# Optimization experiments

Measured on AMD Instinct MI355X. Metric: run time of the kernel, lower is better.

The kernel has to match this reference:

```python
import jax, jax.numpy as jnp
import numpy as np

PALACE_N = 64   # base palace mask size
PALACE_BLOCK = 8  # 8 palaces of 8 positions each


def _palace_base():
    # base 64x64 mask: 1.0 within a palace (8x8 diagonal blocks), 0.5 across palaces
    pid = jnp.arange(PALACE_N) // PALACE_BLOCK
    intra = pid[:, None] == pid[None, :]
    return jnp.where(intra, 1.0, 0.5).astype(jnp.float32)


def _get_mask(T, inter_palace_weight):
    # tile base mask by index modulo 64 (matches mask[i % 64, j % 64])
    base = _palace_base()
    ii = jnp.arange(T) % PALACE_N
    base_T = base[ii[:, None], ii[None, :]]            # [T, T]
    intra = (base_T == 1.0).astype(jnp.float32)
    inter = (base_T < 1.0).astype(jnp.float32)
    return intra + jax.nn.sigmoid(inter_palace_weight) * inter


def setup_inputs() -> dict:
    key = jax.random.key(0)
    ks = jax.random.split(key, 5)
    B, T, D = 4, 2048, 1024
    x = jax.random.normal(ks[0], (B, T, D), dtype=jnp.float32)
    s = 1.0 / np.sqrt(D)
    Wq = jax.random.normal(ks[1], (D, D), dtype=jnp.float32) * s
    Wk = jax.random.normal(ks[2], (D, D), dtype=jnp.float32) * s
    Wv = jax.random.normal(ks[3], (D, D), dtype=jnp.float32) * s
    inter_palace_weight = jnp.float32(0.1)
    return {"x": x, "Wq": Wq, "Wk": Wk, "Wv": Wv,
            "inter_palace_weight": inter_palace_weight}


def reference(x, Wq, Wk, Wv, inter_palace_weight):
    B, T, D = x.shape
    H = 16
    hd = D // H
    scale = hd ** -0.5
    pmask = _get_mask(T, inter_palace_weight)          # [T, T]
    # torch Linear: x @ W.T
    q = (x @ Wq.T).reshape(B, T, H, hd)
    k = (x @ Wk.T).reshape(B, T, H, hd)
    v = (x @ Wv.T).reshape(B, T, H, hd)
    attn = jnp.einsum('bqhd,bkhd->bhqk', q, k) * scale
    attn = attn * pmask[None, None, :, :]
    attn = jax.nn.softmax(attn, axis=-1)
    attn = jnp.nan_to_num(attn, nan=0.0)
    out = jnp.einsum('bhqk,bkhd->bqhd', attn, v)
    return out.reshape(B, T, D)
```

## Files before the change

### kernel.cpp

```cpp
#include <hip/hip_runtime.h>

typedef unsigned short u16;
typedef unsigned int u32;
typedef short bf16x8 __attribute__((ext_vector_type(8)));
typedef float f32x4 __attribute__((ext_vector_type(4)));
typedef u32 u32x4 __attribute__((ext_vector_type(4)));

#define AS_GLOBAL __attribute__((address_space(1)))
#define AS_LDS __attribute__((address_space(3)))

__device__ __forceinline__ void async16(const void* g, void* l) {
  __builtin_amdgcn_global_load_lds((const AS_GLOBAL u32*)g, (AS_LDS u32*)l, 16, 0, 0);
}

__device__ __forceinline__ u16 f2bf(float f) {
  u32 u = __builtin_bit_cast(u32, f);
  u += 0x7FFFu + ((u >> 16) & 1u);
  return (u16)(u >> 16);
}

__device__ __forceinline__ u32 pk2bf(float lo, float hi) {
  return __builtin_amdgcn_perm(__builtin_bit_cast(u32, hi),
                               __builtin_bit_cast(u32, lo), 0x07060302u);
}

__device__ __forceinline__ float fexp2(float x) {
#if __has_builtin(__builtin_amdgcn_exp2f)
  return __builtin_amdgcn_exp2f(x);
#else
  return exp2f(x);
#endif
}

__global__ __launch_bounds__(256) void cvt_all(const float* __restrict__ x,
                                               const float* __restrict__ wq,
                                               const float* __restrict__ wk,
                                               const float* __restrict__ wv,
                                               u16* __restrict__ xb,
                                               u16* __restrict__ wb) {
  const int blk = blockIdx.x;
  const float* src;
  u16* dst;
  int i;
  if (blk < 8192) {
    src = x; dst = xb; i = blk * 256 + threadIdx.x;
  } else if (blk < 9216) {
    src = wq; dst = wb; i = (blk - 8192) * 256 + threadIdx.x;
  } else if (blk < 10240) {
    src = wk; dst = wb + 1048576; i = (blk - 9216) * 256 + threadIdx.x;
  } else {
    src = wv; dst = wb + 2097152; i = (blk - 10240) * 256 + threadIdx.x;
  }
  float4 f = reinterpret_cast<const float4*>(src)[i];
  ushort4 o;
  o.x = f2bf(f.x); o.y = f2bf(f.y); o.z = f2bf(f.z); o.w = f2bf(f.w);
  reinterpret_cast<ushort4*>(dst)[i] = o;
}

__global__ __launch_bounds__(256, 2) void qkv_gemm(const u16* __restrict__ X,
                                                   const u16* __restrict__ W,
                                                   u16* __restrict__ O) {
  const int z = blockIdx.z;
  const u16* Wz = W + (size_t)z * (1024 * 1024);
  u16* Oz = O + (size_t)z * (8192 * 1024);

  __shared__ __align__(16) u16 SMEM[4][8192];

  const int t = threadIdx.x;
  const int lane = t & 63, w = t >> 6, quad = lane >> 4, lq = lane & 15;
  const int wm = (w >> 1) * 64, wn = (w & 1) * 64;
  const int sw = lq & 7;
  const size_t m0 = (size_t)blockIdx.x * 128;
  const int n0 = blockIdx.y * 128;

  int off[4];
#pragma unroll
  for (int j = 0; j < 4; ++j) {
    const int s = j * 256 + t, row = s >> 3, c = (s & 7) ^ (row & 7);
    off[j] = row * 1024 + c * 8;
  }
  const u16* gA = X + m0 * 1024;
  const u16* gB = Wz + (size_t)n0 * 1024;

  f32x4 acc[4][4];
#pragma unroll
  for (int i = 0; i < 4; ++i)
#pragma unroll
    for (int j = 0; j < 4; ++j) acc[i][j] = f32x4{0.f, 0.f, 0.f, 0.f};

  auto stage = [&](int kt, int nb) {
    const u16* ga = gA + kt * 64;
    const u16* gb = gB + kt * 64;
#pragma unroll
    for (int j = 0; j < 4; ++j)
      async16(ga + off[j], &SMEM[nb][(j * 256 + t) * 8]);
#pragma unroll
    for (int j = 0; j < 4; ++j)
      async16(gb + off[j], &SMEM[2 + nb][(j * 256 + t) * 8]);
  };

  stage(0, 0);

  for (int kt = 0; kt < 16; ++kt) {
    const int cur = kt & 1;
    __syncthreads();
    if (kt < 15) stage(kt + 1, cur ^ 1);

    bf16x8 Af[4][2], Bf[4][2];
#pragma unroll
    for (int i = 0; i < 4; ++i)
#pragma unroll
      for (int ks = 0; ks < 2; ++ks) {
        Af[i][ks] = *reinterpret_cast<const bf16x8*>(
            &SMEM[cur][(wm + i * 16 + lq) * 64 + ((ks * 4 + quad) ^ sw) * 8]);
        Bf[i][ks] = *reinterpret_cast<const bf16x8*>(
            &SMEM[2 + cur][(wn + i * 16 + lq) * 64 + ((ks * 4 + quad) ^ sw) * 8]);
      }
#pragma unroll
    for (int i = 0; i < 4; ++i)
#pragma unroll
      for (int j = 0; j < 4; ++j) {
        acc[i][j] = __builtin_amdgcn_mfma_f32_16x16x32_bf16(Af[i][0], Bf[j][0], acc[i][j], 0, 0, 0);
        acc[i][j] = __builtin_amdgcn_mfma_f32_16x16x32_bf16(Af[i][1], Bf[j][1], acc[i][j], 0, 0, 0);
      }
  }

  __syncthreads();
  u16* ep = &SMEM[w][0];
  if (z != 2) {
#pragma unroll
    for (int i = 0; i < 4; ++i)
#pragma unroll
      for (int j = 0; j < 4; ++j)
#pragma unroll
        for (int r = 0; r < 4; ++r)
          ep[(i * 16 + quad * 4 + r) * 80 + j * 16 + lq] = f2bf(acc[i][j][r]);
  } else {
#pragma unroll
    for (int i = 0; i < 4; ++i)
#pragma unroll
      for (int j = 0; j < 4; ++j)
#pragma unroll
        for (int r = 0; r < 4; ++r)
          ep[(j * 16 + lq) * 80 + i * 16 + quad * 4 + r] = f2bf(acc[i][j][r]);
  }
  asm volatile("s_waitcnt lgkmcnt(0)" ::: "memory");

  const int r8 = lane >> 3, c8 = lane & 7;
  const size_t ms = m0 + wm;
  const size_t bb = ms >> 11, tt0 = ms & 2047;
  const int hh = (n0 + wn) >> 6;
  if (z != 2) {
    u16* gbase = Oz + ((bb * 16 + hh) * 2048 + tt0) * 64;
#pragma unroll
    for (int kq = 0; kq < 8; ++kq) {
      const int row = kq * 8 + r8;
      bf16x8 v = *reinterpret_cast<const bf16x8*>(&ep[row * 80 + c8 * 8]);
      *reinterpret_cast<bf16x8*>(&gbase[(size_t)row * 64 + c8 * 8]) = v;
    }
  } else {
    u16* gbase = Oz + ((size_t)(bb * 16 + hh) * 64) * 2048 + tt0;
#pragma unroll
    for (int kq = 0; kq < 8; ++kq) {
      const int row = kq * 8 + r8;
      bf16x8 v = *reinterpret_cast<const bf16x8*>(&ep[row * 80 + c8 * 8]);
      *reinterpret_cast<bf16x8*>(&gbase[(size_t)row * 2048 + c8 * 8]) = v;
    }
  }
}

__global__ __launch_bounds__(256, 2) void palace_attn(const u16* __restrict__ Q,
                                                      const u16* __restrict__ K,
                                                      const u16* __restrict__ Vt,
                                                      float* __restrict__ out,
                                                      const float* __restrict__ wptr) {
  const int bh = blockIdx.x, qt = blockIdx.y;
  const int h = bh & 15, b = bh >> 4;
  const size_t base = (size_t)bh * (2048 * 64);

  __shared__ __align__(16) u16 Ks[2][64 * 64];
  __shared__ __align__(16) u16 Vs[2][64 * 64];

  const int t = threadIdx.x;
  const int w = t >> 6, lane = t & 63, quad = lane >> 4, lq = lane & 15;
  const int lq3 = lq >> 3;
  const int swk = (lq & 3) | (((lq >> 2) & 1) << 2);
  const int swv = (lq & 3) | (lq3 << 2);
  const float sig = 1.f / (1.f + __expf(-wptr[0]));
  const float Ci = 0.125f * 1.44269504f;
  const float Co = Ci * sig;
  const float MC = 14.4269504f;

  float cft[2][4];
#pragma unroll
  for (int half = 0; half < 2; ++half)
#pragma unroll
    for (int qg = 0; qg < 4; ++qg)
      cft[half][qg] = (half * 4 + quad == qg * 2 + lq3) ? Ci : Co;

  bf16x8 qf[4][2];
#pragma unroll
  for (int qg = 0; qg < 4; ++qg)
#pragma unroll
    for (int kc = 0; kc < 2; ++kc)
      qf[qg][kc] = *reinterpret_cast<const bf16x8*>(
          Q + base + (size_t)(qt * 256 + w * 64 + qg * 16 + lq) * 64 + kc * 32 + quad * 8);

  int ko[2], vo[2];
#pragma unroll
  for (int r = 0; r < 2; ++r) {
    const int slot = r * 256 + t;
    const int row = slot >> 3;
    const int sr = (row & 3) | (((row >> 3) & 1) << 2);
    const int cl = (slot & 7) ^ sr;
    ko[r] = row * 64 + cl * 8;
    vo[r] = row * 2048 + cl * 8;
  }

  f32x4 O[4][4];
  f32x4 Lacc[4];
#pragma unroll
  for (int qg = 0; qg < 4; ++qg) {
    Lacc[qg] = f32x4{0.f, 0.f, 0.f, 0.f};
#pragma unroll
    for (int dg = 0; dg < 4; ++dg) O[qg][dg] = f32x4{0.f, 0.f, 0.f, 0.f};
  }

  const short oneb = (short)0x3F80;
  const bf16x8 ones8 = {oneb, oneb, oneb, oneb, oneb, oneb, oneb, oneb};

  {
    const u16* kgp = K + base;
    const u16* vgp = Vt + base;
    async16(kgp + ko[0], &Ks[0][(w * 64) * 8]);
    async16(kgp + ko[1], &Ks[0][(256 + w * 64) * 8]);
    async16(vgp + vo[0], &Vs[0][(w * 64) * 8]);
    async16(vgp + vo[1], &Vs[0][(256 + w * 64) * 8]);
  }

  for (int kt = 0; kt < 32; ++kt) {
    const int cur = kt & 1;
    __syncthreads();
    if (kt < 31) {
      const u16* kgp = K + base + (size_t)(kt + 1) * 4096;
      const u16* vgp = Vt + base + (size_t)(kt + 1) * 64;
      const int nb = cur ^ 1;
      async16(kgp + ko[0], &Ks[nb][(w * 64) * 8]);
      async16(kgp + ko[1], &Ks[nb][(256 + w * 64) * 8]);
      async16(vgp + vo[0], &Vs[nb][(w * 64) * 8]);
      async16(vgp + vo[1], &Vs[nb][(256 + w * 64) * 8]);
    }

#pragma unroll
    for (int half = 0; half < 2; ++half) {
      const int rb = half * 32 + ((lq >> 2) << 3) + (lq & 3);
      bf16x8 kf[2][2];
#pragma unroll
      for (int kg2 = 0; kg2 < 2; ++kg2) {
        const int krow = rb + kg2 * 4;
        kf[kg2][0] = *reinterpret_cast<const bf16x8*>(
            &Ks[cur][krow * 64 + (quad ^ swk) * 8]);
        kf[kg2][1] = *reinterpret_cast<const bf16x8*>(
            &Ks[cur][krow * 64 + ((quad + 4) ^ swk) * 8]);
      }

      bf16x8 vbf[4];
#pragma unroll
      for (int dg = 0; dg < 4; ++dg)
        vbf[dg] = *reinterpret_cast<const bf16x8*>(
            &Vs[cur][(dg * 16 + lq) * 64 + ((half * 4 + quad) ^ swv) * 8]);

#pragma unroll
      for (int qg = 0; qg < 4; ++qg) {
        f32x4 z0 = {0.f, 0.f, 0.f, 0.f}, z1 = {0.f, 0.f, 0.f, 0.f};
        z0 = __builtin_amdgcn_mfma_f32_16x16x32_bf16(kf[0][0], qf[qg][0], z0, 0, 0, 0);
        z0 = __builtin_amdgcn_mfma_f32_16x16x32_bf16(kf[0][1], qf[qg][1], z0, 0, 0, 0);
        z1 = __builtin_amdgcn_mfma_f32_16x16x32_bf16(kf[1][0], qf[qg][0], z1, 0, 0, 0);
        z1 = __builtin_amdgcn_mfma_f32_16x16x32_bf16(kf[1][1], qf[qg][1], z1, 0, 0, 0);

        const float cf = cft[half][qg];
        const float p0 = fexp2(__builtin_fmaf(z0[0], cf, -MC));
        const float p1 = fexp2(__builtin_fmaf(z0[1], cf, -MC));
        const float p2 = fexp2(__builtin_fmaf(z0[2], cf, -MC));
        const float p3 = fexp2(__builtin_fmaf(z0[3], cf, -MC));
        const float p4 = fexp2(__builtin_fmaf(z1[0], cf, -MC));
        const float p5 = fexp2(__builtin_fmaf(z1[1], cf, -MC));
        const float p6 = fexp2(__builtin_fmaf(z1[2], cf, -MC));
        const float p7 = fexp2(__builtin_fmaf(z1[3], cf, -MC));

        u32x4 pk;
        pk.x = pk2bf(p0, p1);
        pk.y = pk2bf(p2, p3);
        pk.z = pk2bf(p4, p5);
        pk.w = pk2bf(p6, p7);
        const bf16x8 pa = __builtin_bit_cast(bf16x8, pk);

        Lacc[qg] = __builtin_amdgcn_mfma_f32_16x16x32_bf16(pa, ones8, Lacc[qg], 0, 0, 0);
#pragma unroll
        for (int dg = 0; dg < 4; ++dg)
          O[qg][dg] = __builtin_amdgcn_mfma_f32_16x16x32_bf16(pa, vbf[dg], O[qg][dg], 0, 0, 0);
      }
    }
  }

#pragma unroll
  for (int qg = 0; qg < 4; ++qg) {
#pragma unroll
    for (int r = 0; r < 4; ++r) {
      const float iv = 1.f / Lacc[qg][r];
      const size_t trow = (size_t)(qt * 256 + w * 64 + qg * 16 + quad * 4 + r);
      float* op = out + ((size_t)b * 2048 + trow) * 1024 + h * 64 + lq;
#pragma unroll
      for (int dg = 0; dg < 4; ++dg) op[dg * 16] = O[qg][dg][r] * iv;
    }
  }
}

extern "C" void kernel_launch(void* const* d_in, const int* in_sizes, int n_in,
                              void* d_out, int out_size, void* d_ws, size_t ws_size,
                              hipStream_t stream) {
  (void)in_sizes; (void)n_in; (void)out_size; (void)ws_size;
  const float* x = (const float*)d_in[0];
  const float* Wq = (const float*)d_in[1];
  const float* Wk = (const float*)d_in[2];
  const float* Wv = (const float*)d_in[3];
  const float* wip = (const float*)d_in[4];
  float* out = (float*)d_out;

  u16* xb = (u16*)d_ws;
  u16* wb = xb + 8388608;
  u16* qb = wb + 3145728;
  u16* kb = qb + 8388608;
  u16* vb = kb + 8388608;

  cvt_all<<<11264, 256, 0, stream>>>(x, Wq, Wk, Wv, xb, wb);
  qkv_gemm<<<dim3(64, 8, 3), 256, 0, stream>>>(xb, wb, qb);
  palace_attn<<<dim3(64, 8, 1), 256, 0, stream>>>(qb, kb, vb, out, wip);
}
```

Before: 216.9 us.

## Split attention block across eight waves with 32 query rows each

Each attention block now runs 512 threads (8 waves), and every wave handles 32 query rows instead of 64. With twice the threads, each thread issues one async K and one async V load per tile instead of two. The aim is more waves in flight to hide latency and spread the K/V loads. The cost is that each wave rereads the same K/V fragments from LDS while doing half as much MFMA work on them, so LDS read traffic per FLOP doubles. The per-wave palace-mask coefficient selection was adjusted to match the new query offset.

Result: faster. 211.7 us (-2.4%).

```diff
diff --git a/kernel.cpp b/kernel.cpp
--- a/kernel.cpp
+++ b/kernel.cpp
@@ -169,7 +169,7 @@
   }
 }
 
-__global__ __launch_bounds__(256, 2) void palace_attn(const u16* __restrict__ Q,
+__global__ __launch_bounds__(512, 4) void palace_attn(const u16* __restrict__ Q,
                                                       const u16* __restrict__ K,
                                                       const u16* __restrict__ Vt,
                                                       float* __restrict__ out,
@@ -191,36 +191,32 @@
   const float Co = Ci * sig;
   const float MC = 14.4269504f;
 
-  float cft[2][4];
+  const int qs0 = (w & 1) * 4;
+  float cft[2][2];
 #pragma unroll
   for (int half = 0; half < 2; ++half)
 #pragma unroll
-    for (int qg = 0; qg < 4; ++qg)
-      cft[half][qg] = (half * 4 + quad == qg * 2 + lq3) ? Ci : Co;
-
-  bf16x8 qf[4][2];
-#pragma unroll
-  for (int qg = 0; qg < 4; ++qg)
+    for (int qg = 0; qg < 2; ++qg)
+      cft[half][qg] = (half * 4 + quad == qs0 + qg * 2 + lq3) ? Ci : Co;
+
+  bf16x8 qf[2][2];
+#pragma unroll
+  for (int qg = 0; qg < 2; ++qg)
 #pragma unroll
     for (int kc = 0; kc < 2; ++kc)
       qf[qg][kc] = *reinterpret_cast<const bf16x8*>(
-          Q + base + (size_t)(qt * 256 + w * 64 + qg * 16 + lq) * 64 + kc * 32 + quad * 8);
-
-  int ko[2], vo[2];
-#pragma unroll
-  for (int r = 0; r < 2; ++r) {
-    const int slot = r * 256 + t;
-    const int row = slot >> 3;
-    const int sr = (row & 3) | (((row >> 3) & 1) << 2);
-    const int cl = (slot & 7) ^ sr;
-    ko[r] = row * 64 + cl * 8;
-    vo[r] = row * 2048 + cl * 8;
-  }
-
-  f32x4 O[4][4];
-  f32x4 Lacc[4];
-#pragma unroll
-  for (int qg = 0; qg < 4; ++qg) {
+          Q + base + (size_t)(qt * 256 + w * 32 + qg * 16 + lq) * 64 + kc * 32 + quad * 8);
+
+  const int row_s = t >> 3;
+  const int sr_s = (row_s & 3) | (((row_s >> 3) & 1) << 2);
+  const int cl_s = (t & 7) ^ sr_s;
+  const int ko = row_s * 64 + cl_s * 8;
+  const int vo = row_s * 2048 + cl_s * 8;
+
+  f32x4 O[2][4];
+  f32x4 Lacc[2];
+#pragma unroll
+  for (int qg = 0; qg < 2; ++qg) {
     Lacc[qg] = f32x4{0.f, 0.f, 0.f, 0.f};
 #pragma unroll
     for (int dg = 0; dg < 4; ++dg) O[qg][dg] = f32x4{0.f, 0.f, 0.f, 0.f};
@@ -232,10 +228,8 @@
   {
     const u16* kgp = K + base;
     const u16* vgp = Vt + base;
-    async16(kgp + ko[0], &Ks[0][(w * 64) * 8]);
-    async16(kgp + ko[1], &Ks[0][(256 + w * 64) * 8]);
-    async16(vgp + vo[0], &Vs[0][(w * 64) * 8]);
-    async16(vgp + vo[1], &Vs[0][(256 + w * 64) * 8]);
+    async16(kgp + ko, &Ks[0][(w * 64) * 8]);
+    async16(vgp + vo, &Vs[0][(w * 64) * 8]);
   }
 
   for (int kt = 0; kt < 32; ++kt) {
@@ -245,10 +239,8 @@
       const u16* kgp = K + base + (size_t)(kt + 1) * 4096;
       const u16* vgp = Vt + base + (size_t)(kt + 1) * 64;
       const int nb = cur ^ 1;
-      async16(kgp + ko[0], &Ks[nb][(w * 64) * 8]);
-      async16(kgp + ko[1], &Ks[nb][(256 + w * 64) * 8]);
-      async16(vgp + vo[0], &Vs[nb][(w * 64) * 8]);
-      async16(vgp + vo[1], &Vs[nb][(256 + w * 64) * 8]);
+      async16(kgp + ko, &Ks[nb][(w * 64) * 8]);
+      async16(vgp + vo, &Vs[nb][(w * 64) * 8]);
     }
 
 #pragma unroll
@@ -271,7 +263,7 @@
             &Vs[cur][(dg * 16 + lq) * 64 + ((half * 4 + quad) ^ swv) * 8]);
 
 #pragma unroll
-      for (int qg = 0; qg < 4; ++qg) {
+      for (int qg = 0; qg < 2; ++qg) {
         f32x4 z0 = {0.f, 0.f, 0.f, 0.f}, z1 = {0.f, 0.f, 0.f, 0.f};
         z0 = __builtin_amdgcn_mfma_f32_16x16x32_bf16(kf[0][0], qf[qg][0], z0, 0, 0, 0);
         z0 = __builtin_amdgcn_mfma_f32_16x16x32_bf16(kf[0][1], qf[qg][1], z0, 0, 0, 0);
@@ -304,11 +296,11 @@
   }
 
 #pragma unroll
-  for (int qg = 0; qg < 4; ++qg) {
+  for (int qg = 0; qg < 2; ++qg) {
 #pragma unroll
     for (int r = 0; r < 4; ++r) {
       const float iv = 1.f / Lacc[qg][r];
-      const size_t trow = (size_t)(qt * 256 + w * 64 + qg * 16 + quad * 4 + r);
+      const size_t trow = (size_t)(qt * 256 + w * 32 + qg * 16 + quad * 4 + r);
       float* op = out + ((size_t)b * 2048 + trow) * 1024 + h * 64 + lq;
 #pragma unroll
       for (int dg = 0; dg < 4; ++dg) op[dg * 16] = O[qg][dg][r] * iv;
@@ -335,5 +327,5 @@
 
   cvt_all<<<11264, 256, 0, stream>>>(x, Wq, Wk, Wv, xb, wb);
   qkv_gemm<<<dim3(64, 8, 3), 256, 0, stream>>>(xb, wb, qb);
-  palace_attn<<<dim3(64, 8, 1), 256, 0, stream>>>(qb, kb, vb, out, wip);
-}
+  palace_attn<<<dim3(64, 8, 1), 512, 0, stream>>>(qb, kb, vb, out, wip);
+}
```
